# Kernel tuning notes

Hardware: AMD Instinct MI355X
Metric: run time of the kernel (lower is better)

## Reference

```python
import jax, jax.numpy as jnp
import numpy as np
import math

B, T, C = 4, 2048, 1024
N_HEAD = 16
HEAD_DIM = C // N_HEAD


def setup_inputs() -> dict:
    key = jax.random.key(0)
    k1, k2, k3, k4, k5 = jax.random.split(key, 5)
    s = 1.0 / math.sqrt(C)
    return {
        "x": jax.random.normal(k1, (B, T, C), dtype=jnp.float32),
        "W_attn": jax.random.normal(k2, (3 * C, C), dtype=jnp.float32) * s,
        "b_attn": jax.random.normal(k3, (3 * C,), dtype=jnp.float32) * 0.02,
        "W_proj": jax.random.normal(k4, (C, C), dtype=jnp.float32) * s,
        "b_proj": jax.random.normal(k5, (C,), dtype=jnp.float32) * 0.02,
    }


def reference(x, W_attn, b_attn, W_proj, b_proj):
    Bx, Tx, Cx = x.shape
    # QKV projection (torch Linear: x @ W.T + b), split into q,k,v
    qkv = jnp.einsum("btc,dc->btd", x, W_attn) + b_attn  # [B,T,3C]
    q, k, v = jnp.split(qkv, 3, axis=-1)
    # [B,T,C] -> [B,H,T,hd]
    def to_heads(t):
        return t.reshape(Bx, Tx, N_HEAD, HEAD_DIM).transpose(0, 2, 1, 3)
    q, k, v = to_heads(q), to_heads(k), to_heads(v)
    scale = 1.0 / math.sqrt(HEAD_DIM)
    att = jnp.einsum("bhqd,bhkd->bhqk", q, k) * scale  # [B,H,T,T]
    causal = jnp.tril(jnp.ones((Tx, Tx), dtype=bool))
    att = jnp.where(causal, att, -jnp.inf)
    att = jax.nn.softmax(att, axis=-1)
    y = jnp.einsum("bhqk,bhkd->bhqd", att, v)  # [B,H,T,hd]
    y = y.transpose(0, 2, 1, 3).reshape(Bx, Tx, Cx)
    y = jnp.einsum("btc,dc->btd", y, W_proj) + b_proj
    return y
```

## Files before the change

### kernel.cpp

```cpp
#include <hip/hip_runtime.h>
#include <hip/hip_bf16.h>
#include <stdint.h>

typedef unsigned short u16;
typedef __attribute__((ext_vector_type(8))) short bf16x8;
typedef __attribute__((ext_vector_type(4))) short s16x4;
typedef __attribute__((ext_vector_type(4))) float f32x4;

#define B_SZ 4
#define T_SZ 2048
#define C_SZ 1024
#define NH   16
#define HD   64
#define LOG2E 1.44269504088896340736f

__device__ __forceinline__ u16 f2bf(float f) {
  unsigned int u = __float_as_uint(f);
  u += 0x7fffu + ((u >> 16) & 1u);
  return (u16)(u >> 16);
}
__device__ __forceinline__ u16 f2bf_hu(float f) {
  return (u16)((__float_as_uint(f) + 0x8000u) >> 16);
}
__device__ __forceinline__ void gload_lds16(const u16* g, u16* l) {
  __builtin_amdgcn_global_load_lds((const __attribute__((address_space(1))) void*)g,
                                   (__attribute__((address_space(3))) void*)l, 16, 0, 0);
}

__global__ void cast_f32_bf16(const float* __restrict__ in, u16* __restrict__ out, int n8) {
  int i = blockIdx.x * blockDim.x + threadIdx.x;
  if (i < n8) {
    const float4* p = (const float4*)in + (size_t)i * 2;
    float4 a = p[0], b = p[1];
    bf16x8 o;
    o[0] = (short)f2bf(a.x); o[1] = (short)f2bf(a.y);
    o[2] = (short)f2bf(a.z); o[3] = (short)f2bf(a.w);
    o[4] = (short)f2bf(b.x); o[5] = (short)f2bf(b.y);
    o[6] = (short)f2bf(b.z); o[7] = (short)f2bf(b.w);
    ((bf16x8*)out)[i] = o;
  }
}

template <int MODE>
__launch_bounds__(512, 2)
__global__ void gemm8(const u16* __restrict__ A, const u16* __restrict__ Bw,
                      const float* __restrict__ bias,
                      void* __restrict__ O0, void* __restrict__ O1, void* __restrict__ O2,
                      int M, int N, int K) {
  extern __shared__ u16 lds[];
  u16* As = lds;
  u16* Bs = lds + 32768;
  const int tid = threadIdx.x;
  const int lane = tid & 63, w = tid >> 6;
  const int wm = w >> 2, wn = w & 3;
  const int quad = lane >> 4, l16 = lane & 15;

  const int gx = gridDim.x;
  const int nwg = gx * gridDim.y;
  const int wg0 = blockIdx.y * gx + blockIdx.x;
  const int swz = (wg0 & 7) * (nwg >> 3) + (wg0 >> 3);
  const int n0 = (swz % gx) * 256;
  const int m0 = (swz / gx) * 256;

  const int dr8 = lane >> 3;
  const int dc8 = (lane & 7) ^ dr8;
  const u16* gAL = A + (size_t)(m0 + w * 8 + dr8) * K + dc8 * 8;
  const u16* gBL = Bw + (size_t)(n0 + w * 8 + dr8) * K + dc8 * 8;
  u16* dA = As + w * 512;
  u16* dB = Bs + w * 512;

  const int NT = K >> 6;

  auto stageA = [&](int tile) {
    u16* d = dA + (tile & 1) * 16384;
    const u16* g = gAL + (size_t)tile * 64;
#pragma unroll
    for (int h = 0; h < 2; ++h)
#pragma unroll
      for (int i = 0; i < 2; ++i)
        gload_lds16(g + (size_t)(h * 128 + i * 64) * K, d + h * 8192 + i * 4096);
  };
  auto stageB = [&](int tile, int h) {
    u16* d = dB + (tile & 1) * 16384 + h * 8192;
    const u16* g = gBL + (size_t)tile * 64 + (size_t)h * 128 * K;
#pragma unroll
    for (int i = 0; i < 2; ++i)
      gload_lds16(g + (size_t)i * 64 * K, d + i * 4096);
  };

  f32x4 acc[8][4];
#pragma unroll
  for (int i = 0; i < 8; i++)
#pragma unroll
    for (int j = 0; j < 4; j++) acc[i][j] = (f32x4){0.f, 0.f, 0.f, 0.f};

  stageA(0);
  stageB(0, 0); stageB(0, 1);
  stageB(1, 0); stageB(1, 1);
  asm volatile("s_waitcnt vmcnt(4)" ::: "memory");
  __builtin_amdgcn_s_barrier();

  const u16* AbaseR = As + wm * 8192;
  const u16* BbaseR = Bs + (wn >> 1) * 8192 + (wn & 1) * 64 * 64;
  const int sK0 = ((quad) ^ (l16 & 7)) * 8;
  const int sK1 = ((4 + quad) ^ (l16 & 7)) * 8;

  const int NIT = NT >> 1;
  for (int j = 0; j < NIT; ++j) {
#pragma unroll
    for (int tt = 0; tt < 2; ++tt) {
      const int tile = 2 * j + tt;
      const int bufo = (tile & 1) * 16384;
      const u16* Ab = AbaseR + bufo;
      const u16* Bb = BbaseR + bufo;
      bf16x8 bfr[4][2];
#pragma unroll
      for (int mp = 0; mp < 4; ++mp) {
        bf16x8 af[2][2];
#pragma unroll
        for (int a2 = 0; a2 < 2; ++a2) {
          const int ro = ((mp * 2 + a2) * 16 + l16) * 64;
          af[a2][0] = *(const bf16x8*)&Ab[ro + sK0];
          af[a2][1] = *(const bf16x8*)&Ab[ro + sK1];
        }
        if (mp == 0) {
#pragma unroll
          for (int nt = 0; nt < 4; ++nt) {
            const int ro = (nt * 16 + l16) * 64;
            bfr[nt][0] = *(const bf16x8*)&Bb[ro + sK0];
            bfr[nt][1] = *(const bf16x8*)&Bb[ro + sK1];
          }
        }
        if (mp == 0) { if (tile + 1 < NT) stageA(tile + 1); }
        else if (mp == 1) { if (tile + 2 < NT) stageB(tile + 2, 0); }
        else if (mp == 2) { if (tile + 2 < NT) stageB(tile + 2, 1); }
        if (mp == 0) asm volatile("s_waitcnt lgkmcnt(8)");
        asm volatile("" ::: "memory");
        __builtin_amdgcn_s_barrier();
        asm volatile("s_waitcnt lgkmcnt(0)" ::: "memory");
        __builtin_amdgcn_sched_barrier(0);
        __builtin_amdgcn_s_setprio(1);
#pragma unroll
        for (int a2 = 0; a2 < 2; ++a2)
#pragma unroll
          for (int nt = 0; nt < 4; ++nt) {
            f32x4 c = acc[mp * 2 + a2][nt];
            c = __builtin_amdgcn_mfma_f32_16x16x32_bf16(af[a2][0], bfr[nt][0], c, 0, 0, 0);
            c = __builtin_amdgcn_mfma_f32_16x16x32_bf16(af[a2][1], bfr[nt][1], c, 0, 0, 0);
            acc[mp * 2 + a2][nt] = c;
          }
        __builtin_amdgcn_s_setprio(0);
        if (mp == 3) {
          if (tile + 2 >= NT) asm volatile("s_waitcnt vmcnt(0)" ::: "memory");
          else                asm volatile("s_waitcnt vmcnt(4)" ::: "memory");
        }
        asm volatile("" ::: "memory");
        __builtin_amdgcn_s_barrier();
      }
    }
  }

  float bv[4];
#pragma unroll
  for (int nt = 0; nt < 4; nt++) bv[nt] = bias[n0 + wn * 64 + nt * 16 + l16];

  if (MODE == 0) {
    float* Cout = (float*)O0;
#pragma unroll
    for (int mt = 0; mt < 8; mt++) {
      const int row = m0 + wm * 128 + mt * 16 + quad * 4;
#pragma unroll
      for (int nt = 0; nt < 4; nt++) {
        const int col = n0 + wn * 64 + nt * 16 + l16;
#pragma unroll
        for (int r = 0; r < 4; r++)
          Cout[(size_t)(row + r) * N + col] = acc[mt][nt][r] + bv[nt];
      }
    }
  } else {
    const int nsec = (n0 + wn * 64) >> 10;
    const int hh = ((n0 + wn * 64) >> 6) & 15;
    if (nsec < 2) {
      u16* dst = (u16*)(nsec == 0 ? O0 : O1);
#pragma unroll
      for (int mt = 0; mt < 8; mt++) {
        const int row = m0 + wm * 128 + mt * 16 + quad * 4;
        const int bb = row >> 11;
        const int t = row & 2047;
#pragma unroll
        for (int nt = 0; nt < 4; nt++) {
          const int dh = nt * 16 + l16;
          const size_t a = (((size_t)bb * NH + hh) * T_SZ + t) * HD + dh;
#pragma unroll
          for (int r = 0; r < 4; r++)
            dst[a + (size_t)r * HD] = f2bf(acc[mt][nt][r] + bv[nt]);
        }
      }
    } else {
      u16* vth = (u16*)O2;
#pragma unroll
      for (int mt = 0; mt < 8; mt++) {
        const int row = m0 + wm * 128 + mt * 16 + quad * 4;
        const int bb = row >> 11;
        const int t = row & 2047;
#pragma unroll
        for (int nt = 0; nt < 4; nt++) {
          const int dh = nt * 16 + l16;
          s16x4 pk;
#pragma unroll
          for (int r = 0; r < 4; r++) pk[r] = (short)f2bf(acc[mt][nt][r] + bv[nt]);
          *(s16x4*)&vth[(((size_t)bb * NH + hh) * HD + dh) * T_SZ + t] = pk;
        }
      }
    }
  }
}

__device__ __forceinline__ void attn_step(
    int kb, int kbn, int w, int quad, int l16, int qt128, int sw0, int sw1,
    const u16* gK0, const u16* gK1, const u16* gV0, const u16* gV1,
    u16* KsF, u16* VsF, u16* PsW,
    const bf16x8 (&qf)[2][2], f32x4 (&o)[2][4], float (&l_i)[2][4]) {
  __syncthreads();

  if (kb + 1 < kbn) {
    const int nb = (kb + 1) & 1;
    const size_t ko = (size_t)(kb + 1) * 64 * HD;
    const int vo = (kb + 1) * 64;
    gload_lds16(gK0 + ko, KsF + nb * 4096 + (2 * w) * 512);
    gload_lds16(gK1 + ko, KsF + nb * 4096 + (2 * w + 1) * 512);
    gload_lds16(gV0 + vo, VsF + nb * 4096 + (2 * w) * 512);
    gload_lds16(gV1 + vo, VsF + nb * 4096 + (2 * w + 1) * 512);
  }

  const u16* Kb = KsF + (kb & 1) * 4096;
  const u16* Vb = VsF + (kb & 1) * 4096;
  const int kt0 = kb * 64;
  const float SC = 0.125f * LOG2E;

#pragma unroll
  for (int m = 0; m < 2; m++) {
    const int mrow = qt128 + w * 32 + m * 16;
    const int qr = mrow + quad * 4;
    const bool diag = (kt0 + 64 > mrow);

    f32x4 s[4];
    __builtin_amdgcn_s_setprio(1);
#pragma unroll
    for (int nt = 0; nt < 4; nt++) {
      bf16x8 kf0 = *(const bf16x8*)&Kb[(nt * 16 + l16) * 64 + sw0];
      bf16x8 kf1 = *(const bf16x8*)&Kb[(nt * 16 + l16) * 64 + sw1];
      f32x4 t0 = (f32x4){0.f, 0.f, 0.f, 0.f};
      t0 = __builtin_amdgcn_mfma_f32_16x16x32_bf16(qf[m][0], kf0, t0, 0, 0, 0);
      t0 = __builtin_amdgcn_mfma_f32_16x16x32_bf16(qf[m][1], kf1, t0, 0, 0, 0);
      s[nt] = t0;
    }
    __builtin_amdgcn_s_setprio(0);

    if (diag) {
#pragma unroll
      for (int nt = 0; nt < 4; nt++) {
        const int dk = kt0 + nt * 16 + l16 - qr;
#pragma unroll
        for (int r = 0; r < 4; r++) {
          float v = (dk > r) ? -10000.f : s[nt][r] * SC;
          s[nt][r] = exp2f(v);
        }
      }
    } else {
#pragma unroll
      for (int nt = 0; nt < 4; nt++)
#pragma unroll
        for (int r = 0; r < 4; r++)
          s[nt][r] = exp2f(s[nt][r] * SC);
    }
#pragma unroll
    for (int r = 0; r < 4; r++)
      l_i[m][r] += (s[0][r] + s[1][r]) + (s[2][r] + s[3][r]);

#pragma unroll
    for (int nt = 0; nt < 4; nt++)
#pragma unroll
      for (int r = 0; r < 4; r++)
        PsW[(quad * 4 + r) * 72 + nt * 16 + l16] = f2bf_hu(s[nt][r]);
    bf16x8 p0 = *(const bf16x8*)&PsW[l16 * 72 + quad * 8];
    bf16x8 p1 = *(const bf16x8*)&PsW[l16 * 72 + 32 + quad * 8];
    __builtin_amdgcn_s_setprio(1);
#pragma unroll
    for (int nt = 0; nt < 4; nt++) {
      bf16x8 v0 = *(const bf16x8*)&Vb[(nt * 16 + l16) * 64 + sw0];
      bf16x8 v1 = *(const bf16x8*)&Vb[(nt * 16 + l16) * 64 + sw1];
      o[m][nt] = __builtin_amdgcn_mfma_f32_16x16x32_bf16(p0, v0, o[m][nt], 0, 0, 0);
      o[m][nt] = __builtin_amdgcn_mfma_f32_16x16x32_bf16(p1, v1, o[m][nt], 0, 0, 0);
    }
    __builtin_amdgcn_s_setprio(0);
  }
}

__launch_bounds__(256, 3)
__global__ void attn_fused(const u16* __restrict__ qh, const u16* __restrict__ kh,
                           const u16* __restrict__ vth, u16* __restrict__ out) {
  __shared__ __align__(16) u16 Ks[2][64 * 64];
  __shared__ __align__(16) u16 Vs[2][64 * 64];
  __shared__ __align__(16) u16 Ps[4][16 * 72];
  const int qt = 15 - blockIdx.z;
  const int h = blockIdx.x, b = blockIdx.y;
  const int tid = threadIdx.x;
  const int lane = tid & 63, w = tid >> 6;
  const int quad = lane >> 4, l16 = lane & 15;
  const size_t bh = (size_t)b * NH + h;
  const u16* Kbase = kh + bh * T_SZ * HD;
  const u16* Vbase = vth + bh * HD * T_SZ;
  const int qt128 = qt * 128;

  const int dr = lane >> 3;
  const int dc = (lane & 7) ^ dr;
  const u16* gK0 = Kbase + (size_t)(2 * w * 8 + dr) * HD + dc * 8;
  const u16* gK1 = Kbase + (size_t)((2 * w + 1) * 8 + dr) * HD + dc * 8;
  const u16* gV0 = Vbase + (size_t)(2 * w * 8 + dr) * T_SZ + dc * 8;
  const u16* gV1 = Vbase + (size_t)((2 * w + 1) * 8 + dr) * T_SZ + dc * 8;
  u16* KsF = &Ks[0][0];
  u16* VsF = &Vs[0][0];
  u16* PsW = &Ps[w][0];

  bf16x8 qf[2][2];
#pragma unroll
  for (int m = 0; m < 2; m++) {
    const int t = qt128 + w * 32 + m * 16 + l16;
    const u16* qrow = qh + (bh * T_SZ + t) * HD;
    qf[m][0] = *(const bf16x8*)(qrow + quad * 8);
    qf[m][1] = *(const bf16x8*)(qrow + 32 + quad * 8);
  }

  f32x4 o[2][4];
  float l_i[2][4];
#pragma unroll
  for (int m = 0; m < 2; m++)
#pragma unroll
    for (int i = 0; i < 4; i++) {
      o[m][i] = (f32x4){0.f, 0.f, 0.f, 0.f};
      l_i[m][i] = 0.f;
    }

  const int kbn = 2 * qt + 2;
  const int sw0 = (quad ^ (l16 & 7)) * 8;
  const int sw1 = ((4 + quad) ^ (l16 & 7)) * 8;

  gload_lds16(gK0, KsF + (2 * w) * 512);
  gload_lds16(gK1, KsF + (2 * w + 1) * 512);
  gload_lds16(gV0, VsF + (2 * w) * 512);
  gload_lds16(gV1, VsF + (2 * w + 1) * 512);

  for (int kb = 0; kb < kbn; kb++)
    attn_step(kb, kbn, w, quad, l16, qt128, sw0, sw1,
              gK0, gK1, gV0, gV1, KsF, VsF, PsW, qf, o, l_i);

#pragma unroll
  for (int m = 0; m < 2; m++)
#pragma unroll
    for (int r = 0; r < 4; r++) {
      float v = l_i[m][r];
      v += __shfl_xor(v, 1);
      v += __shfl_xor(v, 2);
      v += __shfl_xor(v, 4);
      v += __shfl_xor(v, 8);
      const float inv = 1.f / v;
      const int t = qt128 + w * 32 + m * 16 + quad * 4 + r;
      const size_t orow = ((size_t)b * T_SZ + t) * C_SZ + (size_t)h * HD;
#pragma unroll
      for (int nt = 0; nt < 4; nt++)
        out[orow + nt * 16 + l16] = f2bf(o[m][nt][r] * inv);
    }
}

extern "C" void kernel_launch(void* const* d_in, const int* in_sizes, int n_in,
                              void* d_out, int out_size, void* d_ws, size_t ws_size,
                              hipStream_t stream) {
  (void)in_sizes; (void)n_in; (void)out_size; (void)ws_size;
  const float* x      = (const float*)d_in[0];
  const float* W_attn = (const float*)d_in[1];
  const float* b_attn = (const float*)d_in[2];
  const float* W_proj = (const float*)d_in[3];
  const float* b_proj = (const float*)d_in[4];
  float* out = (float*)d_out;

  char* ws = (char*)d_ws;
  u16* xb  = (u16*)ws;  ws += (size_t)8192 * 1024 * 2;
  u16* Wab = (u16*)ws;  ws += (size_t)3072 * 1024 * 2;
  u16* Wpb = (u16*)ws;  ws += (size_t)1024 * 1024 * 2;
  u16* qhb = (u16*)ws;  ws += (size_t)8192 * 1024 * 2;
  u16* khb = (u16*)ws;  ws += (size_t)8192 * 1024 * 2;
  u16* vtb = (u16*)ws;  ws += (size_t)8192 * 1024 * 2;
  u16* aob = (u16*)ws;

  dim3 blk(256);
  cast_f32_bf16<<<(8192 * 1024 / 8 + 255) / 256, blk, 0, stream>>>(x, xb, 8192 * 1024 / 8);
  cast_f32_bf16<<<(3072 * 1024 / 8 + 255) / 256, blk, 0, stream>>>(W_attn, Wab, 3072 * 1024 / 8);
  cast_f32_bf16<<<(1024 * 1024 / 8 + 255) / 256, blk, 0, stream>>>(W_proj, Wpb, 1024 * 1024 / 8);

  gemm8<1><<<dim3(3072 / 256, 8192 / 256), dim3(512), 131072, stream>>>(
      xb, Wab, b_attn, qhb, khb, vtb, 8192, 3072, 1024);
  attn_fused<<<dim3(NH, B_SZ, 16), blk, 0, stream>>>(qhb, khb, vtb, aob);
  gemm8<0><<<dim3(1024 / 256, 8192 / 256), dim3(512), 131072, stream>>>(
      aob, Wpb, b_proj, out, nullptr, nullptr, 8192, 1024, 1024);
}
```

Measured before the change: 266.3 us.

## Use smaller-tile GEMM for output projection and hoist K/V fragment loads

```diff
diff --git a/kernel.cpp b/kernel.cpp
--- a/kernel.cpp
+++ b/kernel.cpp
@@ -41,12 +41,78 @@
   }
 }
 
-template <int MODE>
+__launch_bounds__(256, 3)
+__global__ void gemm_bt0(const u16* __restrict__ A, const u16* __restrict__ Bw,
+                         const float* __restrict__ bias, float* __restrict__ Cout,
+                         int M, int N, int K) {
+  __shared__ __align__(16) u16 As[128 * 32];
+  __shared__ __align__(16) u16 Bs[128 * 32];
+  const int tid = threadIdx.x;
+  const int lane = tid & 63;
+  const int w = tid >> 6;
+  const int wr = w >> 1, wc = w & 1;
+  const int quad = lane >> 4, l16 = lane & 15;
+  const int m0 = blockIdx.y * 128;
+  const int n0 = blockIdx.x * 128;
+
+  const int srow = lane >> 2;
+  const int scol = (lane & 3) * 8;
+  const u16* gA = A + (size_t)(m0 + w * 32 + srow) * K + scol;
+  const u16* gB = Bw + (size_t)(n0 + w * 32 + srow) * K + scol;
+  u16* lA0 = &As[(w * 32) * 32];
+  u16* lA1 = &As[(w * 32 + 16) * 32];
+  u16* lB0 = &Bs[(w * 32) * 32];
+  u16* lB1 = &Bs[(w * 32 + 16) * 32];
+  const size_t rstep = (size_t)16 * K;
+
+  f32x4 acc[4][4];
+#pragma unroll
+  for (int i = 0; i < 4; i++)
+#pragma unroll
+    for (int j = 0; j < 4; j++) acc[i][j] = (f32x4){0.f, 0.f, 0.f, 0.f};
+
+  for (int k0 = 0; k0 < K; k0 += 32) {
+    __syncthreads();
+    gload_lds16(gA + k0, lA0);
+    gload_lds16(gA + rstep + k0, lA1);
+    gload_lds16(gB + k0, lB0);
+    gload_lds16(gB + rstep + k0, lB1);
+    __syncthreads();
+    bf16x8 af[4], bfr[4];
+#pragma unroll
+    for (int mt = 0; mt < 4; mt++)
+      af[mt] = *(const bf16x8*)&As[(wr * 64 + mt * 16 + l16) * 32 + quad * 8];
+#pragma unroll
+    for (int nt = 0; nt < 4; nt++)
+      bfr[nt] = *(const bf16x8*)&Bs[(wc * 64 + nt * 16 + l16) * 32 + quad * 8];
+#pragma unroll
+    for (int mt = 0; mt < 4; mt++)
+#pragma unroll
+      for (int nt = 0; nt < 4; nt++)
+        acc[mt][nt] = __builtin_amdgcn_mfma_f32_16x16x32_bf16(af[mt], bfr[nt], acc[mt][nt], 0, 0, 0);
+  }
+
+  float bv[4];
+#pragma unroll
+  for (int nt = 0; nt < 4; nt++) bv[nt] = bias[n0 + wc * 64 + nt * 16 + l16];
+#pragma unroll
+  for (int mt = 0; mt < 4; mt++) {
+    const int row = m0 + wr * 64 + mt * 16 + quad * 4;
+#pragma unroll
+    for (int nt = 0; nt < 4; nt++) {
+      const int col = n0 + wc * 64 + nt * 16 + l16;
+#pragma unroll
+      for (int r = 0; r < 4; r++)
+        Cout[(size_t)(row + r) * N + col] = acc[mt][nt][r] + bv[nt];
+    }
+  }
+}
+
 __launch_bounds__(512, 2)
-__global__ void gemm8(const u16* __restrict__ A, const u16* __restrict__ Bw,
-                      const float* __restrict__ bias,
-                      void* __restrict__ O0, void* __restrict__ O1, void* __restrict__ O2,
-                      int M, int N, int K) {
+__global__ void gemm8_qkv(const u16* __restrict__ A, const u16* __restrict__ Bw,
+                          const float* __restrict__ bias,
+                          u16* __restrict__ O0, u16* __restrict__ O1, u16* __restrict__ O2,
+                          int M, int N, int K) {
   extern __shared__ u16 lds[];
   u16* As = lds;
   u16* Bs = lds + 32768;
@@ -164,53 +230,38 @@
 #pragma unroll
   for (int nt = 0; nt < 4; nt++) bv[nt] = bias[n0 + wn * 64 + nt * 16 + l16];
 
-  if (MODE == 0) {
-    float* Cout = (float*)O0;
+  const int nsec = (n0 + wn * 64) >> 10;
+  const int hh = ((n0 + wn * 64) >> 6) & 15;
+  if (nsec < 2) {
+    u16* dst = (nsec == 0 ? O0 : O1);
 #pragma unroll
     for (int mt = 0; mt < 8; mt++) {
       const int row = m0 + wm * 128 + mt * 16 + quad * 4;
+      const int bb = row >> 11;
+      const int t = row & 2047;
 #pragma unroll
       for (int nt = 0; nt < 4; nt++) {
-        const int col = n0 + wn * 64 + nt * 16 + l16;
+        const int dh = nt * 16 + l16;
+        const size_t a = (((size_t)bb * NH + hh) * T_SZ + t) * HD + dh;
 #pragma unroll
         for (int r = 0; r < 4; r++)
-          Cout[(size_t)(row + r) * N + col] = acc[mt][nt][r] + bv[nt];
+          dst[a + (size_t)r * HD] = f2bf(acc[mt][nt][r] + bv[nt]);
       }
     }
   } else {
-    const int nsec = (n0 + wn * 64) >> 10;
-    const int hh = ((n0 + wn * 64) >> 6) & 15;
-    if (nsec < 2) {
-      u16* dst = (u16*)(nsec == 0 ? O0 : O1);
-#pragma unroll
-      for (int mt = 0; mt < 8; mt++) {
-        const int row = m0 + wm * 128 + mt * 16 + quad * 4;
-        const int bb = row >> 11;
-        const int t = row & 2047;
-#pragma unroll
-        for (int nt = 0; nt < 4; nt++) {
-          const int dh = nt * 16 + l16;
-          const size_t a = (((size_t)bb * NH + hh) * T_SZ + t) * HD + dh;
-#pragma unroll
-          for (int r = 0; r < 4; r++)
-            dst[a + (size_t)r * HD] = f2bf(acc[mt][nt][r] + bv[nt]);
-        }
-      }
-    } else {
-      u16* vth = (u16*)O2;
-#pragma unroll
-      for (int mt = 0; mt < 8; mt++) {
-        const int row = m0 + wm * 128 + mt * 16 + quad * 4;
-        const int bb = row >> 11;
-        const int t = row & 2047;
-#pragma unroll
-        for (int nt = 0; nt < 4; nt++) {
-          const int dh = nt * 16 + l16;
-          s16x4 pk;
-#pragma unroll
-          for (int r = 0; r < 4; r++) pk[r] = (short)f2bf(acc[mt][nt][r] + bv[nt]);
-          *(s16x4*)&vth[(((size_t)bb * NH + hh) * HD + dh) * T_SZ + t] = pk;
-        }
+    u16* vth = O2;
+#pragma unroll
+    for (int mt = 0; mt < 8; mt++) {
+      const int row = m0 + wm * 128 + mt * 16 + quad * 4;
+      const int bb = row >> 11;
+      const int t = row & 2047;
+#pragma unroll
+      for (int nt = 0; nt < 4; nt++) {
+        const int dh = nt * 16 + l16;
+        s16x4 pk;
+#pragma unroll
+        for (int r = 0; r < 4; r++) pk[r] = (short)f2bf(acc[mt][nt][r] + bv[nt]);
+        *(s16x4*)&vth[(((size_t)bb * NH + hh) * HD + dh) * T_SZ + t] = pk;
       }
     }
   }
@@ -238,6 +289,16 @@
   const int kt0 = kb * 64;
   const float SC = 0.125f * LOG2E;
 
+  bf16x8 kf[4][2], vf[4][2];
+#pragma unroll
+  for (int nt = 0; nt < 4; nt++) {
+    const int ro = (nt * 16 + l16) * 64;
+    kf[nt][0] = *(const bf16x8*)&Kb[ro + sw0];
+    kf[nt][1] = *(const bf16x8*)&Kb[ro + sw1];
+    vf[nt][0] = *(const bf16x8*)&Vb[ro + sw0];
+    vf[nt][1] = *(const bf16x8*)&Vb[ro + sw1];
+  }
+
 #pragma unroll
   for (int m = 0; m < 2; m++) {
     const int mrow = qt128 + w * 32 + m * 16;
@@ -248,11 +309,9 @@
     __builtin_amdgcn_s_setprio(1);
 #pragma unroll
     for (int nt = 0; nt < 4; nt++) {
-      bf16x8 kf0 = *(const bf16x8*)&Kb[(nt * 16 + l16) * 64 + sw0];
-      bf16x8 kf1 = *(const bf16x8*)&Kb[(nt * 16 + l16) * 64 + sw1];
       f32x4 t0 = (f32x4){0.f, 0.f, 0.f, 0.f};
-      t0 = __builtin_amdgcn_mfma_f32_16x16x32_bf16(qf[m][0], kf0, t0, 0, 0, 0);
-      t0 = __builtin_amdgcn_mfma_f32_16x16x32_bf16(qf[m][1], kf1, t0, 0, 0, 0);
+      t0 = __builtin_amdgcn_mfma_f32_16x16x32_bf16(qf[m][0], kf[nt][0], t0, 0, 0, 0);
+      t0 = __builtin_amdgcn_mfma_f32_16x16x32_bf16(qf[m][1], kf[nt][1], t0, 0, 0, 0);
       s[nt] = t0;
     }
     __builtin_amdgcn_s_setprio(0);
@@ -288,10 +347,8 @@
     __builtin_amdgcn_s_setprio(1);
 #pragma unroll
     for (int nt = 0; nt < 4; nt++) {
-      bf16x8 v0 = *(const bf16x8*)&Vb[(nt * 16 + l16) * 64 + sw0];
-      bf16x8 v1 = *(const bf16x8*)&Vb[(nt * 16 + l16) * 64 + sw1];
-      o[m][nt] = __builtin_amdgcn_mfma_f32_16x16x32_bf16(p0, v0, o[m][nt], 0, 0, 0);
-      o[m][nt] = __builtin_amdgcn_mfma_f32_16x16x32_bf16(p1, v1, o[m][nt], 0, 0, 0);
+      o[m][nt] = __builtin_amdgcn_mfma_f32_16x16x32_bf16(p0, vf[nt][0], o[m][nt], 0, 0, 0);
+      o[m][nt] = __builtin_amdgcn_mfma_f32_16x16x32_bf16(p1, vf[nt][1], o[m][nt], 0, 0, 0);
     }
     __builtin_amdgcn_s_setprio(0);
   }
@@ -398,9 +455,9 @@
   cast_f32_bf16<<<(3072 * 1024 / 8 + 255) / 256, blk, 0, stream>>>(W_attn, Wab, 3072 * 1024 / 8);
   cast_f32_bf16<<<(1024 * 1024 / 8 + 255) / 256, blk, 0, stream>>>(W_proj, Wpb, 1024 * 1024 / 8);
 
-  gemm8<1><<<dim3(3072 / 256, 8192 / 256), dim3(512), 131072, stream>>>(
+  gemm8_qkv<<<dim3(3072 / 256, 8192 / 256), dim3(512), 131072, stream>>>(
       xb, Wab, b_attn, qhb, khb, vtb, 8192, 3072, 1024);
   attn_fused<<<dim3(NH, B_SZ, 16), blk, 0, stream>>>(qhb, khb, vtb, aob);
-  gemm8<0><<<dim3(1024 / 256, 8192 / 256), dim3(512), 131072, stream>>>(
-      aob, Wpb, b_proj, out, nullptr, nullptr, 8192, 1024, 1024);
-}
+  gemm_bt0<<<dim3(1024 / 128, 8192 / 128), blk, 0, stream>>>(
+      aob, Wpb, b_proj, out, 8192, 1024, 1024);
+}
```

Result: slower. 307.5 us (+15.5%).
